# Kernel tuning notes

Hardware: AMD Instinct MI355X
Metric: run time of the kernel (lower is better)

Reference implementation:

```python
import jax, jax.numpy as jnp
import numpy as np

BIG = 1.0e6  # sentinel 'infinite' 1D distance (BIG**2 = 1e12 is safely finite in fp32)


def _edt_sq(zero_mask):
    """Exact squared Euclidean distance transform to nearest True in zero_mask.

    Two-pass separable exact EDT (matches scipy.ndimage.distance_transform_edt):
      pass 1: 1-D distance along W via forward/backward cummax scans
      pass 2: min-plus over H: D2[i,j] = min_k g2[k,j] + (i-k)^2
    zero_mask: [H, W] bool (True where the source array equals 0).
    """
    H, W = zero_mask.shape
    col = jnp.arange(W, dtype=jnp.float32)
    # index of last zero to the left / first zero to the right
    last = jax.lax.cummax(jnp.where(zero_mask, col, -BIG), axis=1)
    nxt = -jax.lax.cummax(jnp.where(zero_mask, -col, -BIG), axis=1, reverse=True)
    g = jnp.minimum(jnp.minimum(col - last, nxt - col), BIG)  # [H, W] 1-D dist
    g2 = g * g
    row = jnp.arange(H, dtype=jnp.float32)
    sq = (row[:, None] - row[None, :]) ** 2  # [H, H]
    # D2[i, j] = min_k g2[k, j] + (i - k)^2  -- exact 2-D squared EDT
    return jnp.min(g2[None, :, :] + sq[:, :, None], axis=1)


def _distance_map(mask):
    """Signed distance map: EDT(mask) - EDT(1 - mask); zeros if mask empty."""
    pos = jnp.sqrt(_edt_sq(mask == 0))   # dist of foreground px to nearest background
    neg = jnp.sqrt(_edt_sq(mask != 0))   # dist of background px to nearest foreground
    d = pos - neg
    return jnp.where(mask.sum() == 0, jnp.zeros_like(d), d)


def boundary_loss(pred, target):
    B, C, H, W = pred.shape
    masks = target.reshape(B * C, H, W)
    # sequence over B*C to keep the [H,H,W] min-plus intermediate per-image
    dmaps = jax.lax.map(_distance_map, masks).reshape(B, C, H, W)
    # sum_c mean_{b,h,w}(sig(pred_c)*d_c) / C  ==  overall mean
    return jnp.mean(jax.nn.sigmoid(pred) * dmaps)


def setup_inputs() -> dict:
    key = jax.random.key(0)
    k1, k2 = jax.random.split(key)
    pred = jax.random.normal(k1, (8, 3, 256, 256), dtype=jnp.float32)
    target = jax.random.randint(k2, (8, 3, 256, 256), 0, 2, dtype=jnp.int32)
    return {"pred": pred, "target": target}


def reference(pred, target):
    return boundary_loss(pred, target)
```

## Files before the change

kernel.cpp:

```cpp
#include <hip/hip_runtime.h>
#include <math.h>

#define NIMG 24
#define H    256
#define W    256
#define NPIX (H * W)
#define NROWS (NIMG * H)
#define CPB  16
#define GRID2 (NIMG * (W / CPB))
#define NPART GRID2
#define BIGF 1.0e6f
#define CAPTHR (-5.0e5f)

__device__ __forceinline__ float wscan_fwd_max(float v, int lane) {
#pragma unroll
    for (int off = 1; off < 64; off <<= 1) {
        float u = __shfl_up(v, off, 64);
        if (lane >= off) v = fmaxf(v, u);
    }
    return v;
}
__device__ __forceinline__ float wscan_rev_min(float v, int lane) {
#pragma unroll
    for (int off = 1; off < 64; off <<= 1) {
        float u = __shfl_down(v, off, 64);
        if (lane + off < 64) v = fminf(v, u);
    }
    return v;
}

__global__ void edt_rows_kernel(const int* __restrict__ tgt,
                                float* __restrict__ f) {
    const int tid  = blockIdx.x * 256 + threadIdx.x;
    const int gw   = tid >> 6;
    const int lane = tid & 63;
    const int img  = gw >> 8;
    const int row  = gw & 255;

    const int4 tv = ((const int4*)(tgt + (img << 16) + (row << 8)))[lane];
    const float c0 = (float)(lane << 2);
    const float c1 = c0 + 1.0f, c2 = c0 + 2.0f, c3 = c0 + 3.0f;

    const int prevw = __shfl_up(tv.w, 1, 64);
    const bool ch0 = (lane > 0) && ((tv.x != 0) != (prevw != 0));
    const bool ch1 = (tv.y != 0) != (tv.x != 0);
    const bool ch2 = (tv.z != 0) != (tv.y != 0);
    const bool ch3 = (tv.w != 0) != (tv.z != 0);

    const float a0 = ch0 ? c0 : -BIGF;
    const float a1 = ch1 ? c1 : a0;
    const float a2 = ch2 ? c2 : a1;
    const float a3 = ch3 ? c3 : a2;
    const float sm = wscan_fwd_max(a3, lane);
    float ex = __shfl_up(sm, 1, 64);
    if (lane == 0) ex = -BIGF;
    const float s0 = fmaxf(ex, a0);
    const float s1 = fmaxf(ex, a1);
    const float s2 = fmaxf(ex, a2);
    const float s3 = fmaxf(ex, a3);

    const float rb3 = ch3 ? c3 : BIGF;
    const float rb2 = ch2 ? c2 : rb3;
    const float rb1 = ch1 ? c1 : rb2;
    const float rb0 = ch0 ? c0 : rb1;
    const float sr  = wscan_rev_min(rb0, lane);
    float exr = __shfl_down(sr, 1, 64);
    if (lane == 63) exr = BIGF;
    const float n0 = fminf(rb1, exr);
    const float n1 = fminf(rb2, exr);
    const float n2 = fminf(rb3, exr);
    const float n3 = exr;

    const float g0 = fminf(fminf(c0 - s0 + 1.0f, n0 - c0), BIGF);
    const float g1 = fminf(fminf(c1 - s1 + 1.0f, n1 - c1), BIGF);
    const float g2 = fminf(fminf(c2 - s2 + 1.0f, n2 - c2), BIGF);
    const float g3 = fminf(fminf(c3 - s3 + 1.0f, n3 - c3), BIGF);

    float4 o;
    o.x = (tv.x != 0) ? g0 : -g0;
    o.y = (tv.y != 0) ? g1 : -g1;
    o.z = (tv.z != 0) ? g2 : -g2;
    o.w = (tv.w != 0) ? g3 : -g3;
    ((float4*)(f + (img << 16) + (row << 8)))[lane] = o;
}

__global__ void edt_cols_kernel(const float* __restrict__ f,
                                const float* __restrict__ pred,
                                double* __restrict__ partials) {
    const int bid  = blockIdx.x;
    const int img  = bid >> 4;
    const int j0   = (bid & 15) << 4;
    const int t    = threadIdx.x;
    const int lane = t & 63;
    const int wid  = t >> 6;

    __shared__ float sf[H][CPB];
    __shared__ double wsum[4];
    __shared__ int nonempty;
    if (t == 0) nonempty = 0;
    __syncthreads();

    bool myne = false;
#pragma unroll
    for (int s = 0; s < 4; ++s) {
        const int id  = t + (s << 8);
        const int row = id >> 2;
        const int q   = (id & 3) << 2;
        const float4 v = *(const float4*)(f + (img << 16) + (row << 8) + j0 + q);
        *(float4*)&sf[row][q] = v;
        myne = myne || (v.x > CAPTHR) || (v.y > CAPTHR) ||
                       (v.z > CAPTHR) || (v.w > CAPTHR);
    }
    if (myne) nonempty = 1;
    __syncthreads();
    const int flag = nonempty;

    const int c  = t & 15;
    const int r0 = (t >> 4) << 4;
    double acc = 0.0;
#pragma unroll 4
    for (int ii = 0; ii < 16; ++ii) {
        const int i = r0 + ii;
        const float fv = sf[i][c];
        const bool  m  = fv > 0.0f;
        const float sgn = m ? 1.0f : -1.0f;
        const float gi = fabsf(fv);
        const int  gii = (int)gi;
        int lo = i - gii; lo = lo > 0 ? lo : 0;
        int hi = i + gii; hi = hi < (H - 1) ? hi : (H - 1);

        float dm = 3.0e38f;
        float dk = (float)(i - lo);
        for (int k = lo; k <= hi; ++k) {
            const float g = fmaxf(sgn * sf[k][c], 0.0f);
            dm = fminf(dm, g * g + dk * dk);
            dk -= 1.0f;
        }

        float d = m ? sqrtf(dm) : -sqrtf(dm);
        if (!flag) d = 0.0f;
        const float p = pred[(img << 16) + (i << 8) + j0 + c];
        const float sig = 1.0f / (1.0f + expf(-p));
        acc += (double)sig * (double)d;
    }

#pragma unroll
    for (int off = 32; off > 0; off >>= 1) acc += __shfl_down(acc, off, 64);
    if (lane == 0) wsum[wid] = acc;
    __syncthreads();
    if (t == 0) partials[bid] = (wsum[0] + wsum[1]) + (wsum[2] + wsum[3]);
}

__global__ void finalize_kernel(const double* __restrict__ partials,
                                float* __restrict__ out) {
    const int t = threadIdx.x;
    double a = 0.0;
#pragma unroll
    for (int s = 0; s < NPART / 64; ++s) a += partials[t + (s << 6)];
#pragma unroll
    for (int off = 32; off > 0; off >>= 1) a += __shfl_down(a, off, 64);
    if (t == 0) out[0] = (float)(a / (double)(NIMG * NPIX));
}

extern "C" void kernel_launch(void* const* d_in, const int* in_sizes, int n_in,
                              void* d_out, int out_size, void* d_ws, size_t ws_size,
                              hipStream_t stream) {
    const float* pred = (const float*)d_in[0];
    const int*   tgt  = (const int*)d_in[1];
    float* out = (float*)d_out;

    char* ws = (char*)d_ws;
    const size_t fbytes = (size_t)NIMG * NPIX * sizeof(float);
    float*  fbuf     = (float*)(ws);
    double* partials = (double*)(ws + fbytes);

    edt_rows_kernel<<<NROWS / 4, 256, 0, stream>>>(tgt, fbuf);
    edt_cols_kernel<<<GRID2, 256, 0, stream>>>(fbuf, pred, partials);
    finalize_kernel<<<1, 64, 0, stream>>>(partials, out);
}
```

Baseline: 28.33 us.

## Replace row scans with ballot lookup and halve column tile width

The row pass drops the two 6-step shuffle scans. It now finds the nearest change-lane on each side with a single ballot plus clz/ctz and one shuffle each, computing in integers. The column pass uses 8-column tiles instead of 16, which doubles the grid to 768 blocks, and pads shared memory to a stride of 9 to avoid bank conflicts. The cost is more blocks with less work each, scalar shared-memory stores instead of float4, and a finalize kernel whose fixed loop now covers twice as many partials.

Measured after the change: 25.58 us. 1.11x faster.

```diff
diff --git a/kernel.cpp b/kernel.cpp
--- a/kernel.cpp
+++ b/kernel.cpp
@@ -6,28 +6,13 @@
 #define W    256
 #define NPIX (H * W)
 #define NROWS (NIMG * H)
-#define CPB  16
+#define CPB  8
+#define LDP  9
 #define GRID2 (NIMG * (W / CPB))
 #define NPART GRID2
+#define BIGI 1000000
 #define BIGF 1.0e6f
 #define CAPTHR (-5.0e5f)
-
-__device__ __forceinline__ float wscan_fwd_max(float v, int lane) {
-#pragma unroll
-    for (int off = 1; off < 64; off <<= 1) {
-        float u = __shfl_up(v, off, 64);
-        if (lane >= off) v = fmaxf(v, u);
-    }
-    return v;
-}
-__device__ __forceinline__ float wscan_rev_min(float v, int lane) {
-#pragma unroll
-    for (int off = 1; off < 64; off <<= 1) {
-        float u = __shfl_down(v, off, 64);
-        if (lane + off < 64) v = fminf(v, u);
-    }
-    return v;
-}
 
 __global__ void edt_rows_kernel(const int* __restrict__ tgt,
                                 float* __restrict__ f) {
@@ -38,8 +23,7 @@
     const int row  = gw & 255;
 
     const int4 tv = ((const int4*)(tgt + (img << 16) + (row << 8)))[lane];
-    const float c0 = (float)(lane << 2);
-    const float c1 = c0 + 1.0f, c2 = c0 + 2.0f, c3 = c0 + 3.0f;
+    const int c0 = lane << 2;
 
     const int prevw = __shfl_up(tv.w, 1, 64);
     const bool ch0 = (lane > 0) && ((tv.x != 0) != (prevw != 0));
@@ -47,34 +31,47 @@
     const bool ch2 = (tv.z != 0) != (tv.y != 0);
     const bool ch3 = (tv.w != 0) != (tv.z != 0);
 
-    const float a0 = ch0 ? c0 : -BIGF;
-    const float a1 = ch1 ? c1 : a0;
-    const float a2 = ch2 ? c2 : a1;
-    const float a3 = ch3 ? c3 : a2;
-    const float sm = wscan_fwd_max(a3, lane);
-    float ex = __shfl_up(sm, 1, 64);
-    if (lane == 0) ex = -BIGF;
-    const float s0 = fmaxf(ex, a0);
-    const float s1 = fmaxf(ex, a1);
-    const float s2 = fmaxf(ex, a2);
-    const float s3 = fmaxf(ex, a3);
+    const int a0 = ch0 ? c0     : -BIGI;
+    const int a1 = ch1 ? c0 + 1 : a0;
+    const int a2 = ch2 ? c0 + 2 : a1;
+    const int a3 = ch3 ? c0 + 3 : a2;
+    const int rb3 = ch3 ? c0 + 3 : BIGI;
+    const int rb2 = ch2 ? c0 + 2 : rb3;
+    const int rb1 = ch1 ? c0 + 1 : rb2;
+    const int rb0 = ch0 ? c0     : rb1;
 
-    const float rb3 = ch3 ? c3 : BIGF;
-    const float rb2 = ch2 ? c2 : rb3;
-    const float rb1 = ch1 ? c1 : rb2;
-    const float rb0 = ch0 ? c0 : rb1;
-    const float sr  = wscan_rev_min(rb0, lane);
-    float exr = __shfl_down(sr, 1, 64);
-    if (lane == 63) exr = BIGF;
-    const float n0 = fminf(rb1, exr);
-    const float n1 = fminf(rb2, exr);
-    const float n2 = fminf(rb3, exr);
-    const float n3 = exr;
+    const unsigned long long mask = __ballot(ch0 | ch1 | ch2 | ch3);
+    const unsigned long long lowm = mask & ((1ULL << lane) - 1ULL);
+    const unsigned long long him  = (lane < 63) ? (mask >> (lane + 1)) : 0ULL;
 
-    const float g0 = fminf(fminf(c0 - s0 + 1.0f, n0 - c0), BIGF);
-    const float g1 = fminf(fminf(c1 - s1 + 1.0f, n1 - c1), BIGF);
-    const float g2 = fminf(fminf(c2 - s2 + 1.0f, n2 - c2), BIGF);
-    const float g3 = fminf(fminf(c3 - s3 + 1.0f, n3 - c3), BIGF);
+    const int plane = 63 - __builtin_clzll(lowm | 1ULL);
+    const int sh_a  = __shfl(a3, plane & 63, 64);
+    const int ex    = (lowm != 0ULL) ? sh_a : -BIGI;
+
+    const int qlane = lane + 1 +
+        (int)__builtin_ctzll(him | 0x8000000000000000ULL);
+    const int sh_r  = __shfl(rb0, qlane & 63, 64);
+    const int exr   = (him != 0ULL) ? sh_r : BIGI;
+
+    const int s0 = (ex > a0) ? ex : a0;
+    const int s1 = (ex > a1) ? ex : a1;
+    const int s2 = (ex > a2) ? ex : a2;
+    const int s3 = (ex > a3) ? ex : a3;
+    const int n0 = (rb1 < exr) ? rb1 : exr;
+    const int n1 = (rb2 < exr) ? rb2 : exr;
+    const int n2 = (rb3 < exr) ? rb3 : exr;
+    const int n3 = exr;
+
+    auto gcalc = [](int c, int s, int n) -> int {
+        int dp = c - s + 1;
+        int dn = n - c;
+        int g = dp < dn ? dp : dn;
+        return g < BIGI ? g : BIGI;
+    };
+    const float g0 = (float)gcalc(c0,     s0, n0);
+    const float g1 = (float)gcalc(c0 + 1, s1, n1);
+    const float g2 = (float)gcalc(c0 + 2, s2, n2);
+    const float g3 = (float)gcalc(c0 + 3, s3, n3);
 
     float4 o;
     o.x = (tv.x != 0) ? g0 : -g0;
@@ -88,13 +85,13 @@
                                 const float* __restrict__ pred,
                                 double* __restrict__ partials) {
     const int bid  = blockIdx.x;
-    const int img  = bid >> 4;
-    const int j0   = (bid & 15) << 4;
+    const int img  = bid >> 5;
+    const int j0   = (bid & 31) << 3;
     const int t    = threadIdx.x;
     const int lane = t & 63;
     const int wid  = t >> 6;
 
-    __shared__ float sf[H][CPB];
+    __shared__ float sf[H][LDP];
     __shared__ double wsum[4];
     __shared__ int nonempty;
     if (t == 0) nonempty = 0;
@@ -102,12 +99,13 @@
 
     bool myne = false;
 #pragma unroll
-    for (int s = 0; s < 4; ++s) {
+    for (int s = 0; s < 2; ++s) {
         const int id  = t + (s << 8);
-        const int row = id >> 2;
-        const int q   = (id & 3) << 2;
+        const int row = id >> 1;
+        const int q   = (id & 1) << 2;
         const float4 v = *(const float4*)(f + (img << 16) + (row << 8) + j0 + q);
-        *(float4*)&sf[row][q] = v;
+        sf[row][q]     = v.x;  sf[row][q + 1] = v.y;
+        sf[row][q + 2] = v.z;  sf[row][q + 3] = v.w;
         myne = myne || (v.x > CAPTHR) || (v.y > CAPTHR) ||
                        (v.z > CAPTHR) || (v.w > CAPTHR);
     }
@@ -115,11 +113,11 @@
     __syncthreads();
     const int flag = nonempty;
 
-    const int c  = t & 15;
-    const int r0 = (t >> 4) << 4;
+    const int c  = t & 7;
+    const int r0 = (t >> 3) << 3;
     double acc = 0.0;
-#pragma unroll 4
-    for (int ii = 0; ii < 16; ++ii) {
+#pragma unroll
+    for (int ii = 0; ii < 8; ++ii) {
         const int i = r0 + ii;
         const float fv = sf[i][c];
         const bool  m  = fv > 0.0f;
```
